# Performance work log

Measured on AMD Instinct MI355X. Metric: run time of the kernel, lower is better.

Reference implementation:

```python
import jax, jax.numpy as jnp
import numpy as np

PRUNE_RATIO = 0.5
NOISE_SCALE = 0.1
MIXUP_ALPHA = 0.05
TEMPERATURE = 0.5
B, N, D = 32, 4096, 256


def setup_inputs() -> dict:
    key = jax.random.key(0)
    k1, k2, k3 = jax.random.split(key, 3)
    seq = jax.random.normal(k1, (B, N, D), dtype=jnp.float32)
    attn_weights = jax.random.uniform(k2, (B, N), dtype=jnp.float32)
    uniform_noise = jax.random.uniform(k3, (B, N), dtype=jnp.float32)
    return {"seq": seq, "attn_weights": attn_weights, "uniform_noise": uniform_noise}


def reference(seq, attn_weights, uniform_noise):
    b, n, d = seq.shape
    k = max(1, int(n * (1.0 - PRUNE_RATIO)))
    # training branch: gumbel noise from the provided uniform draw
    gumbel = -jnp.log(-jnp.log(uniform_noise + 1e-10) + 1e-10)
    noisy = attn_weights + NOISE_SCALE * gumbel                      # (B, N)
    soft = jax.nn.softmax(noisy / TEMPERATURE, axis=-1)              # (B, N)
    _, top_idx = jax.lax.top_k(soft, k)                              # (B, K) int32
    # gather selected tokens: (B, K, D)
    selected = jnp.take_along_axis(seq, top_idx[:, :, None], axis=1)
    # mixup: mean of the pruned (non-selected) tokens
    mask = jnp.ones((b, n), dtype=seq.dtype).at[
        jnp.arange(b)[:, None], top_idx
    ].set(0.0)                                                       # (B, N), 1 on pruned
    remaining_sum = jnp.einsum('bn,bnd->bd', mask, seq)              # (B, D)
    remaining_count = mask.sum(axis=1, keepdims=True) + 1e-10        # (B, 1)
    remaining_mean = remaining_sum / remaining_count                 # (B, D)
    return selected + MIXUP_ALPHA * remaining_mean[:, None, :]       # (B, K, D)
```

## Files before the change

### kernel.cpp

```cpp
#include <hip/hip_runtime.h>
#include <hip/hip_bf16.h>

#define B_ 32
#define N_ 4096
#define D_ 256
#define K_ 2048
#define RANK_THREADS 512
#define SLICES 8

__global__ __launch_bounds__(RANK_THREADS) void rank_kernel(
    const float* __restrict__ attn, const float* __restrict__ noise,
    int* __restrict__ sortedIdx, float* __restrict__ meanAccum) {
  __shared__ unsigned long long keys[N_];
  const int b = blockIdx.y;
  const int slice = blockIdx.x;
  const int tid = threadIdx.x;

  for (int i = tid; i < N_; i += RANK_THREADS) {
    float u = noise[b * N_ + i];
    float a = attn[b * N_ + i];
    float x = __fadd_rn(u, 1e-10f);
    float l1 = (float)log((double)x);
    float inner = __fadd_rn(-l1, 1e-10f);
    float g = -(float)log((double)inner);
    float noisy = __fadd_rn(a, __fmul_rn(0.1f, g));
    unsigned int fb = __float_as_uint(noisy);
    fb = (fb & 0x80000000u) ? ~fb : (fb | 0x80000000u);
    keys[i] = ((unsigned long long)fb << 32) | (unsigned int)(~i);
  }
  __syncthreads();

  const int i = slice * RANK_THREADS + tid;
  const unsigned long long mine = keys[i];
  const ulonglong2* k2 = (const ulonglong2*)keys;
  unsigned int cnt = 0;
#pragma unroll 16
  for (int j = 0; j < N_ / 2; ++j) {
    ulonglong2 o = k2[j];
    cnt += (o.x > mine) ? 1u : 0u;
    cnt += (o.y > mine) ? 1u : 0u;
  }

  sortedIdx[b * N_ + (int)cnt] = i;

  if (slice == 0 && tid < D_) meanAccum[b * D_ + tid] = 0.0f;
}

__global__ __launch_bounds__(256) void mean_kernel(
    const float* __restrict__ seq, const int* __restrict__ sortedIdx,
    float* __restrict__ meanAccum) {
  const int b = blockIdx.y;
  const int chunk = blockIdx.x;
  const int tid = threadIdx.x;
  const int dv = tid & 63;
  const int sub = tid >> 6;
  const int base = b * N_ + K_ + chunk * 128;

  float4 acc = make_float4(0.f, 0.f, 0.f, 0.f);
  for (int r = sub; r < 128; r += 4) {
    int idx = sortedIdx[base + r];
    const float4* row = (const float4*)(seq + ((size_t)b * N_ + idx) * D_);
    float4 v = row[dv];
    acc.x += v.x; acc.y += v.y; acc.z += v.z; acc.w += v.w;
  }

  __shared__ float4 red[4][64];
  red[sub][dv] = acc;
  __syncthreads();
  if (sub == 0) {
    float4 s0 = red[0][dv], s1 = red[1][dv], s2 = red[2][dv], s3 = red[3][dv];
    float sx = s0.x + s1.x + s2.x + s3.x;
    float sy = s0.y + s1.y + s2.y + s3.y;
    float sz = s0.z + s1.z + s2.z + s3.z;
    float sw = s0.w + s1.w + s2.w + s3.w;
    float* dst = meanAccum + b * D_ + dv * 4;
    atomicAdd(dst + 0, sx);
    atomicAdd(dst + 1, sy);
    atomicAdd(dst + 2, sz);
    atomicAdd(dst + 3, sw);
  }
}

__global__ __launch_bounds__(256) void out_kernel(
    const float* __restrict__ seq, const int* __restrict__ sortedIdx,
    const float* __restrict__ meanAccum, float* __restrict__ out) {
  const unsigned int t = blockIdx.x * 256u + threadIdx.x;
  const int dv = t & 63;
  const int j = (t >> 6) & (K_ - 1);
  const int b = t >> 17;

  int idx = sortedIdx[b * N_ + j];
  float4 v = ((const float4*)(seq + ((size_t)b * N_ + idx) * D_))[dv];
  float4 m = ((const float4*)(meanAccum + b * D_))[dv];
  const float inv_cnt = 1.0f / 2048.0f;
  float4 o;
  o.x = v.x + 0.05f * (m.x * inv_cnt);
  o.y = v.y + 0.05f * (m.y * inv_cnt);
  o.z = v.z + 0.05f * (m.z * inv_cnt);
  o.w = v.w + 0.05f * (m.w * inv_cnt);
  ((float4*)out)[t] = o;
}

extern "C" void kernel_launch(void* const* d_in, const int* in_sizes, int n_in,
                              void* d_out, int out_size, void* d_ws, size_t ws_size,
                              hipStream_t stream) {
  const float* seq  = (const float*)d_in[0];
  const float* attn = (const float*)d_in[1];
  const float* nois = (const float*)d_in[2];
  float* out = (float*)d_out;

  int* sortedIdx   = (int*)d_ws;
  float* meanAccum = (float*)((char*)d_ws + (size_t)B_ * N_ * 4);

  rank_kernel<<<dim3(SLICES, B_), RANK_THREADS, 0, stream>>>(attn, nois, sortedIdx, meanAccum);
  mean_kernel<<<dim3(16, B_), 256, 0, stream>>>(seq, sortedIdx, meanAccum);
  const int total4 = B_ * K_ * (D_ / 4);
  out_kernel<<<total4 / 256, 256, 0, stream>>>(seq, sortedIdx, meanAccum, out);
}
```

Before: 294.1 us.

## Split ranking into key and chunked count kernels with register-blocked comparisons

Computes the sort keys in a separate kernel, then counts ranks by splitting the comparison set into chunks held in shared memory. Each thread compares 8 of its own keys against every chunk key and adds the partial counts to global memory atomically. The mean and output kernels now read each token's rank directly instead of a sorted index list, and the output kernel scatters selected rows to their rank position. This aims to raise reuse of each shared-memory key load and to spread the work over more blocks. The cost is an extra launch, global atomics, and out/mean kernels that scan all N tokens with divergent branches.

```diff
diff --git a/kernel.cpp b/kernel.cpp
--- a/kernel.cpp
+++ b/kernel.cpp
@@ -5,63 +5,89 @@
 #define N_ 4096
 #define D_ 256
 #define K_ 2048
-#define RANK_THREADS 512
-#define SLICES 8
+#define JC_ 8
+#define JCHUNK (N_ / JC_)
+#define CNT_THREADS 512
+#define M_ 8
 
-__global__ __launch_bounds__(RANK_THREADS) void rank_kernel(
+typedef unsigned long long u64;
+typedef unsigned int u32;
+
+__global__ __launch_bounds__(256) void key_kernel(
     const float* __restrict__ attn, const float* __restrict__ noise,
-    int* __restrict__ sortedIdx, float* __restrict__ meanAccum) {
-  __shared__ unsigned long long keys[N_];
+    u64* __restrict__ keys, u32* __restrict__ count,
+    float* __restrict__ meanAccum) {
+  const int t = blockIdx.x * 256 + threadIdx.x;
+  const int i = t & (N_ - 1);
+
+  float u = noise[t];
+  float a = attn[t];
+  float x = __fadd_rn(u, 1e-10f);
+  float l1 = (float)log((double)x);
+  float inner = __fadd_rn(-l1, 1e-10f);
+  float g = -(float)log((double)inner);
+  float noisy = __fadd_rn(a, __fmul_rn(0.1f, g));
+  unsigned int fb = __float_as_uint(noisy);
+  fb = (fb & 0x80000000u) ? ~fb : (fb | 0x80000000u);
+  keys[t] = ((u64)fb << 32) | (u32)(~i);
+
+  count[t] = 0u;
+  if (t < B_ * D_) meanAccum[t] = 0.0f;
+}
+
+__global__ __launch_bounds__(CNT_THREADS) void count_kernel(
+    const u64* __restrict__ keys, u32* __restrict__ count) {
+  __shared__ u64 jk[JCHUNK];
   const int b = blockIdx.y;
-  const int slice = blockIdx.x;
+  const int jc = blockIdx.x;
   const int tid = threadIdx.x;
+  const u64* row = keys + b * N_;
 
-  for (int i = tid; i < N_; i += RANK_THREADS) {
-    float u = noise[b * N_ + i];
-    float a = attn[b * N_ + i];
-    float x = __fadd_rn(u, 1e-10f);
-    float l1 = (float)log((double)x);
-    float inner = __fadd_rn(-l1, 1e-10f);
-    float g = -(float)log((double)inner);
-    float noisy = __fadd_rn(a, __fmul_rn(0.1f, g));
-    unsigned int fb = __float_as_uint(noisy);
-    fb = (fb & 0x80000000u) ? ~fb : (fb | 0x80000000u);
-    keys[i] = ((unsigned long long)fb << 32) | (unsigned int)(~i);
+  jk[tid] = row[jc * JCHUNK + tid];
+
+  u64 mine[M_];
+  u32 cnt[M_];
+#pragma unroll
+  for (int m = 0; m < M_; ++m) {
+    mine[m] = row[m * CNT_THREADS + tid];
+    cnt[m] = 0u;
   }
   __syncthreads();
 
-  const int i = slice * RANK_THREADS + tid;
-  const unsigned long long mine = keys[i];
-  const ulonglong2* k2 = (const ulonglong2*)keys;
-  unsigned int cnt = 0;
-#pragma unroll 16
-  for (int j = 0; j < N_ / 2; ++j) {
+  const ulonglong2* k2 = (const ulonglong2*)jk;
+#pragma unroll 4
+  for (int j = 0; j < JCHUNK / 2; ++j) {
     ulonglong2 o = k2[j];
-    cnt += (o.x > mine) ? 1u : 0u;
-    cnt += (o.y > mine) ? 1u : 0u;
+#pragma unroll
+    for (int m = 0; m < M_; ++m) {
+      cnt[m] += (o.x > mine[m]) ? 1u : 0u;
+      cnt[m] += (o.y > mine[m]) ? 1u : 0u;
+    }
   }
 
-  sortedIdx[b * N_ + (int)cnt] = i;
-
-  if (slice == 0 && tid < D_) meanAccum[b * D_ + tid] = 0.0f;
+  u32* crow = count + b * N_;
+#pragma unroll
+  for (int m = 0; m < M_; ++m) atomicAdd(crow + m * CNT_THREADS + tid, cnt[m]);
 }
 
 __global__ __launch_bounds__(256) void mean_kernel(
-    const float* __restrict__ seq, const int* __restrict__ sortedIdx,
+    const float* __restrict__ seq, const u32* __restrict__ count,
     float* __restrict__ meanAccum) {
   const int b = blockIdx.y;
   const int chunk = blockIdx.x;
   const int tid = threadIdx.x;
   const int dv = tid & 63;
   const int sub = tid >> 6;
-  const int base = b * N_ + K_ + chunk * 128;
+  const int base = chunk * 256;
 
   float4 acc = make_float4(0.f, 0.f, 0.f, 0.f);
-  for (int r = sub; r < 128; r += 4) {
-    int idx = sortedIdx[base + r];
-    const float4* row = (const float4*)(seq + ((size_t)b * N_ + idx) * D_);
-    float4 v = row[dv];
-    acc.x += v.x; acc.y += v.y; acc.z += v.z; acc.w += v.w;
+  for (int r = sub; r < 256; r += 4) {
+    int i = base + r;
+    if (count[b * N_ + i] >= K_) {
+      const float4* rowp = (const float4*)(seq + ((size_t)b * N_ + i) * D_);
+      float4 v = rowp[dv];
+      acc.x += v.x; acc.y += v.y; acc.z += v.z; acc.w += v.w;
+    }
   }
 
   __shared__ float4 red[4][64];
@@ -82,23 +108,25 @@
 }
 
 __global__ __launch_bounds__(256) void out_kernel(
-    const float* __restrict__ seq, const int* __restrict__ sortedIdx,
+    const float* __restrict__ seq, const u32* __restrict__ count,
     const float* __restrict__ meanAccum, float* __restrict__ out) {
   const unsigned int t = blockIdx.x * 256u + threadIdx.x;
   const int dv = t & 63;
-  const int j = (t >> 6) & (K_ - 1);
-  const int b = t >> 17;
+  const int i = (t >> 6) & (N_ - 1);
+  const int b = t >> 18;
 
-  int idx = sortedIdx[b * N_ + j];
-  float4 v = ((const float4*)(seq + ((size_t)b * N_ + idx) * D_))[dv];
-  float4 m = ((const float4*)(meanAccum + b * D_))[dv];
-  const float inv_cnt = 1.0f / 2048.0f;
-  float4 o;
-  o.x = v.x + 0.05f * (m.x * inv_cnt);
-  o.y = v.y + 0.05f * (m.y * inv_cnt);
-  o.z = v.z + 0.05f * (m.z * inv_cnt);
-  o.w = v.w + 0.05f * (m.w * inv_cnt);
-  ((float4*)out)[t] = o;
+  u32 r = count[b * N_ + i];
+  if (r < K_) {
+    float4 v = ((const float4*)(seq + ((size_t)b * N_ + i) * D_))[dv];
+    float4 m = ((const float4*)(meanAccum + b * D_))[dv];
+    const float c = 0.05f / 2048.0f;
+    float4 o;
+    o.x = v.x + c * m.x;
+    o.y = v.y + c * m.y;
+    o.z = v.z + c * m.z;
+    o.w = v.w + c * m.w;
+    ((float4*)out)[((size_t)b * K_ + r) * 64 + dv] = o;
+  }
 }
 
 extern "C" void kernel_launch(void* const* d_in, const int* in_sizes, int n_in,
@@ -109,11 +137,13 @@
   const float* nois = (const float*)d_in[2];
   float* out = (float*)d_out;
 
-  int* sortedIdx   = (int*)d_ws;
-  float* meanAccum = (float*)((char*)d_ws + (size_t)B_ * N_ * 4);
+  u64* keys        = (u64*)d_ws;
+  u32* count       = (u32*)((char*)d_ws + (size_t)B_ * N_ * 8);
+  float* meanAccum = (float*)((char*)d_ws + (size_t)B_ * N_ * 12);
 
-  rank_kernel<<<dim3(SLICES, B_), RANK_THREADS, 0, stream>>>(attn, nois, sortedIdx, meanAccum);
-  mean_kernel<<<dim3(16, B_), 256, 0, stream>>>(seq, sortedIdx, meanAccum);
-  const int total4 = B_ * K_ * (D_ / 4);
-  out_kernel<<<total4 / 256, 256, 0, stream>>>(seq, sortedIdx, meanAccum, out);
+  key_kernel<<<(B_ * N_) / 256, 256, 0, stream>>>(attn, nois, keys, count, meanAccum);
+  count_kernel<<<dim3(JC_, B_), CNT_THREADS, 0, stream>>>(keys, count);
+  mean_kernel<<<dim3(16, B_), 256, 0, stream>>>(seq, count, meanAccum);
+  const int totalT = B_ * N_ * 64;
+  out_kernel<<<totalT / 256, 256, 0, stream>>>(seq, count, meanAccum, out);
 }
```

Result: no change. 291.4 us (-0.9%).
